# Kernel optimization log

Hardware: AMD Instinct MI355X
Metric: run time of the kernel (lower is better)

The kernel has to match this reference:

```python
import jax, jax.numpy as jnp
import numpy as np

N, P, T, D = 25000, 100000, 4, 128
DIN = 4 * D + 4  # 516
LEAKY = 0.001


def setup_inputs() -> dict:
    key = jax.random.key(0)
    ks = jax.random.split(key, 12)
    inp = {
        "coords": jax.random.normal(ks[0], (N, T, 3), jnp.float32),
        "propers": jax.random.randint(ks[1], (P, 4), 0, N, jnp.int64),
        "encoded": jax.random.normal(ks[2], (N, D), jnp.float32),
        "t": jax.random.uniform(ks[3], (T,), jnp.float32),
        "answer": jax.random.normal(ks[4], (N, T, 3), jnp.float32),
        # AggregateMLP(516 -> 128 -> 128 -> 128 -> 2), LeakyReLU(0.001) between
        "W0": jax.random.normal(ks[5], (DIN, D), jnp.float32) / np.sqrt(DIN),
        "b0": jnp.zeros((D,), jnp.float32),
        "W1": jax.random.normal(ks[6], (D, D), jnp.float32) / np.sqrt(D),
        "b1": jnp.zeros((D,), jnp.float32),
        "W2": jax.random.normal(ks[7], (D, D), jnp.float32) / np.sqrt(D),
        "b2": jnp.zeros((D,), jnp.float32),
        "W3": jax.random.normal(ks[8], (D, 2), jnp.float32) / np.sqrt(D),
        "b3": jnp.zeros((2,), jnp.float32),
    }
    return inp


def _forward(coords, propers, encoded, t, answer, W0, b0, W1, b1, W2, b2, W3, b3):
    p0, p1, p2, p3 = propers[:, 0], propers[:, 1], propers[:, 2], propers[:, 3]
    c0, c1, c2, c3 = coords[p0], coords[p1], coords[p2], coords[p3]  # [P,T,3]
    u1 = c1 - c0
    u2 = c2 - c1
    u3 = c3 - c2
    u1xu2 = jnp.cross(u1, u2, axis=-1)
    u2xu3 = jnp.cross(u2, u3, axis=-1)
    u2_norm = jnp.linalg.norm(u2, axis=-1, keepdims=True)
    u1yu2 = u1 * u2_norm
    theta = jnp.arctan2((u1yu2 * u2xu3).sum(-1), (u1xu2 * u2xu3).sum(-1))  # [P,T]
    dr = c0 - c3  # [P,T,3]
    dl = jnp.sqrt(jnp.clip(jnp.square(dr).sum(-1), 1e-12))  # [P,T]
    dh = dr / dl[..., None]

    Pn, Tn = propers.shape[0], t.shape[0]
    bcast = lambda e: jnp.broadcast_to(e[:, None, :], (Pn, Tn, e.shape[-1]))
    feats = jnp.concatenate(
        [
            bcast(encoded[p0]),
            bcast(encoded[p1]),
            bcast(encoded[p2]),
            bcast(encoded[p3]),
            jnp.broadcast_to(t.reshape(1, Tn, 1), (Pn, Tn, 1)),
            jnp.sin(theta)[..., None],
            jnp.cos(theta)[..., None],
            dl[..., None],
        ],
        axis=2,
    )  # [P,T,516]

    h = jax.nn.leaky_relu(feats @ W0 + b0, LEAKY)
    h = jax.nn.leaky_relu(h @ W1 + b1, LEAKY)
    h = jax.nn.leaky_relu(h @ W2 + b2, LEAKY)
    delta = h @ W3 + b3  # [P,T,2]

    out = answer.at[p0].add(-0.5 * delta[:, :, 0:1] * dh)
    out = out.at[p3].add(0.5 * delta[:, :, 1:2] * dh)
    return out


def reference(coords, propers, encoded, t, answer, W0, b0, W1, b1, W2, b2, W3, b3):
    return _forward(coords, propers, encoded, t, answer, W0, b0, W1, b1, W2, b2, W3, b3)
```

## Files before the change

kernel.cpp:

```cpp
#include <hip/hip_runtime.h>
#include <hip/hip_bf16.h>

#define NN 25000
#define PP 100000
#define TT 4
#define DD 128
#define LEAKY 0.001f

#define PB 16
#define ROWS 64

typedef __bf16 bf16;
typedef __bf16 bf16x8 __attribute__((ext_vector_type(8)));
typedef float  f32x4  __attribute__((ext_vector_type(4)));

#define OFF_ENCB  0u
#define OFF_W0SW  6400000u
#define OFF_W1SW  6531072u
#define OFF_W2SW  6563840u
#define OFF_W3SW  6596608u
#define WS_END    6600704u

#define PR_ENCB4 800000
#define PR_W0SW  65536
#define PR_W1SW  16384
#define PR_W2SW  16384
#define PR_W3SW  2048
#define PR_COPY4 75000
#define PR_TOTAL (PR_ENCB4 + PR_W0SW + PR_W1SW + PR_W2SW + PR_W3SW + PR_COPY4)

__global__ __launch_bounds__(256) void prep_kernel(
    const float* __restrict__ encoded, const float* __restrict__ W0,
    const float* __restrict__ W1, const float* __restrict__ W2,
    const float* __restrict__ W3, const float* __restrict__ answer,
    bf16* __restrict__ encB, bf16* __restrict__ W0sw, bf16* __restrict__ W1sw,
    bf16* __restrict__ W2sw, bf16* __restrict__ W3sw, float* __restrict__ out)
{
    int idx = blockIdx.x * 256 + threadIdx.x;
    if (idx < PR_ENCB4) {
        float4 v = ((const float4*)encoded)[idx];
        bf16 pk[4] = {(bf16)v.x, (bf16)v.y, (bf16)v.z, (bf16)v.w};
        *(uint2*)(encB + idx * 4) = *(const uint2*)pk;
        return;
    }
    idx -= PR_ENCB4;
    if (idx < PR_W0SW) {
        int j = idx & 7, lane = (idx >> 3) & 63, c = idx >> 9;
        int fr = lane & 15, quad = lane >> 4;
        int kc = c & 15, iwv = c >> 4;
        int k = kc * 32 + quad * 8 + j;
        W0sw[idx] = (bf16)W0[k * 128 + iwv * 16 + fr];
        return;
    }
    idx -= PR_W0SW;
    if (idx < PR_W1SW) {
        int j = idx & 7, lane = (idx >> 3) & 63, c = idx >> 9;
        int fr = lane & 15, quad = lane >> 4;
        int kc = c & 3, nt = c >> 2;
        int k = kc * 32 + quad * 8 + j;
        W1sw[idx] = (bf16)W1[k * 128 + nt * 16 + fr];
        return;
    }
    idx -= PR_W1SW;
    if (idx < PR_W2SW) {
        int j = idx & 7, lane = (idx >> 3) & 63, c = idx >> 9;
        int fr = lane & 15, quad = lane >> 4;
        int kc = c & 3, nt = c >> 2;
        int k = kc * 32 + quad * 8 + j;
        W2sw[idx] = (bf16)W2[k * 128 + nt * 16 + fr];
        return;
    }
    idx -= PR_W2SW;
    if (idx < PR_W3SW) {
        int j = idx & 7, lane = (idx >> 3) & 63, kc = idx >> 9;
        int fr = lane & 15, quad = lane >> 4;
        int k = kc * 32 + quad * 8 + j;
        W3sw[idx] = (fr < 2) ? (bf16)W3[k * 2 + fr] : (bf16)0.0f;
        return;
    }
    idx -= PR_W3SW;
    if (idx < PR_COPY4) { ((float4*)out)[idx] = ((const float4*)answer)[idx]; }
}

__global__ __launch_bounds__(256, 4) void main_kernel(
    const float* __restrict__ coords, const int* __restrict__ propers,
    const float* __restrict__ tvec, const float* __restrict__ W0,
    const float* __restrict__ b0, const float* __restrict__ b1,
    const float* __restrict__ b2, const float* __restrict__ b3,
    const bf16* __restrict__ encB, const bf16* __restrict__ W0sw,
    const bf16* __restrict__ W1sw, const bf16* __restrict__ W2sw,
    const bf16* __restrict__ W3sw, float* __restrict__ out)
{
    __shared__ bf16 sAH[8704];
    #define SA(p, c) sAH[(p) * 520 + (c)]
    #define SH(r, j) sAH[(r) * 136 + (j)]
    __shared__ int   sNodes[PB][4];
    __shared__ float sSn[ROWS], sCs[ROWS], sDl[ROWS], sDh[ROWS][3];
    __shared__ float sDelta[ROWS][2];

    const int tid  = threadIdx.x;
    const int pBase = blockIdx.x * PB;
    const float tv0 = tvec[0], tv1 = tvec[1], tv2 = tvec[2], tv3 = tvec[3];

    {
        int pair = tid >> 2, sg = tid & 3;
        int p = pair >> 2, i = pair & 3;
        int node = propers[(pBase + p) * 4 + i];
        if (sg == 0) sNodes[p][i] = node;
        const uint4* src = (const uint4*)(encB + (size_t)node * 128 + sg * 32);
        uint4* dst = (uint4*)(&SA(p, i * 128 + sg * 32));
        #pragma unroll
        for (int q = 0; q < 4; ++q) dst[q] = src[q];
    }
    if (tid < ROWS) {
        int r = tid, p = r >> 2, t = r & 3;
        const int* prow = propers + (pBase + p) * 4;
        int n0 = prow[0], n1 = prow[1], n2 = prow[2], n3 = prow[3];
        const float* c0 = coords + n0 * 12 + t * 3;
        const float* c1 = coords + n1 * 12 + t * 3;
        const float* c2 = coords + n2 * 12 + t * 3;
        const float* c3 = coords + n3 * 12 + t * 3;
        float u1x = c1[0]-c0[0], u1y = c1[1]-c0[1], u1z = c1[2]-c0[2];
        float u2x = c2[0]-c1[0], u2y = c2[1]-c1[1], u2z = c2[2]-c1[2];
        float u3x = c3[0]-c2[0], u3y = c3[1]-c2[1], u3z = c3[2]-c2[2];
        float ax = u1y*u2z - u1z*u2y, ay = u1z*u2x - u1x*u2z, az = u1x*u2y - u1y*u2x;
        float bx = u2y*u3z - u2z*u3y, by = u2z*u3x - u2x*u3z, bz = u2x*u3y - u2y*u3x;
        float u2n = sqrtf(u2x*u2x + u2y*u2y + u2z*u2z);
        float num = u2n * (u1x*bx + u1y*by + u1z*bz);
        float den = ax*bx + ay*by + az*bz;
        float hyp = sqrtf(num*num + den*den);
        float sn, cs;
        if (hyp > 1e-30f) { float ih = 1.0f / hyp; sn = num * ih; cs = den * ih; }
        else { sn = 0.0f; cs = 1.0f; }
        float drx = c0[0]-c3[0], dry = c0[1]-c3[1], drz = c0[2]-c3[2];
        float dl = sqrtf(fmaxf(drx*drx + dry*dry + drz*drz, 1e-12f));
        float il = 1.0f / dl;
        sSn[r] = sn; sCs[r] = cs; sDl[r] = dl;
        sDh[r][0] = drx * il; sDh[r][1] = dry * il; sDh[r][2] = drz * il;
    }
    __syncthreads();

    const int wv = tid >> 6, lane = tid & 63;
    const int fr = lane & 15;
    const int quad = lane >> 4;

    f32x4 acc0 = {0.f,0.f,0.f,0.f}, acc1 = {0.f,0.f,0.f,0.f};
    {
        const bf16* aBase = &SA(fr, quad * 8);
        const bf16* w0b = W0sw + (size_t)(wv * 2) * 16 * 512 + lane * 8;
        #pragma unroll
        for (int kc = 0; kc < 16; ++kc) {
            bf16x8 aF = *(const bf16x8*)(aBase + kc * 32);
            bf16x8 bF0 = *(const bf16x8*)(w0b + kc * 512);
            bf16x8 bF1 = *(const bf16x8*)(w0b + (16 + kc) * 512);
            acc0 = __builtin_amdgcn_mfma_f32_16x16x32_bf16(aF, bF0, acc0, 0, 0, 0);
            acc1 = __builtin_amdgcn_mfma_f32_16x16x32_bf16(aF, bF1, acc1, 0, 0, 0);
        }
    }
    __syncthreads();

    #pragma unroll
    for (int i = 0; i < 2; ++i) {
        int j = (wv * 2 + i) * 16 + fr;
        float w512 = W0[512 * 128 + j], w513 = W0[513 * 128 + j];
        float w514 = W0[514 * 128 + j], w515 = W0[515 * 128 + j];
        float bb = b0[j];
        const f32x4 acc = i ? acc1 : acc0;
        #pragma unroll
        for (int reg = 0; reg < 4; ++reg) {
            int p = quad * 4 + reg;
            float g = acc[reg];
            #pragma unroll
            for (int t = 0; t < 4; ++t) {
                int r = p * 4 + t;
                float tvv = (t == 0) ? tv0 : (t == 1) ? tv1 : (t == 2) ? tv2 : tv3;
                float v = g + tvv * w512 + sSn[r] * w513 + sCs[r] * w514 + sDl[r] * w515 + bb;
                v = v > 0.0f ? v : LEAKY * v;
                SH(r, j) = (bf16)v;
            }
        }
    }
    __syncthreads();

    f32x4 hacc[8];
    #pragma unroll
    for (int nt = 0; nt < 8; ++nt) hacc[nt] = (f32x4){0.f,0.f,0.f,0.f};
    {
        const bf16* aRow = &SH(wv * 16 + fr, quad * 8);
        const bf16* w1b = W1sw + lane * 8;
        #pragma unroll
        for (int kc = 0; kc < 4; ++kc) {
            bf16x8 aF = *(const bf16x8*)(aRow + kc * 32);
            #pragma unroll
            for (int nt = 0; nt < 8; ++nt) {
                bf16x8 bF = *(const bf16x8*)(w1b + (nt * 4 + kc) * 512);
                hacc[nt] = __builtin_amdgcn_mfma_f32_16x16x32_bf16(aF, bF, hacc[nt], 0, 0, 0);
            }
        }
    }
    __syncthreads();
    #pragma unroll
    for (int nt = 0; nt < 8; ++nt) {
        int j = nt * 16 + fr;
        float bb = b1[j];
        #pragma unroll
        for (int reg = 0; reg < 4; ++reg) {
            int r = wv * 16 + quad * 4 + reg;
            float v = hacc[nt][reg] + bb;
            v = v > 0.0f ? v : LEAKY * v;
            SH(r, j) = (bf16)v;
        }
    }
    __syncthreads();

    #pragma unroll
    for (int nt = 0; nt < 8; ++nt) hacc[nt] = (f32x4){0.f,0.f,0.f,0.f};
    {
        const bf16* aRow = &SH(wv * 16 + fr, quad * 8);
        const bf16* w2b = W2sw + lane * 8;
        #pragma unroll
        for (int kc = 0; kc < 4; ++kc) {
            bf16x8 aF = *(const bf16x8*)(aRow + kc * 32);
            #pragma unroll
            for (int nt = 0; nt < 8; ++nt) {
                bf16x8 bF = *(const bf16x8*)(w2b + (nt * 4 + kc) * 512);
                hacc[nt] = __builtin_amdgcn_mfma_f32_16x16x32_bf16(aF, bF, hacc[nt], 0, 0, 0);
            }
        }
    }
    __syncthreads();
    #pragma unroll
    for (int nt = 0; nt < 8; ++nt) {
        int j = nt * 16 + fr;
        float bb = b2[j];
        #pragma unroll
        for (int reg = 0; reg < 4; ++reg) {
            int r = wv * 16 + quad * 4 + reg;
            float v = hacc[nt][reg] + bb;
            v = v > 0.0f ? v : LEAKY * v;
            SH(r, j) = (bf16)v;
        }
    }
    __syncthreads();

    {
        f32x4 dacc = {0.f,0.f,0.f,0.f};
        const bf16* aRow = &SH(wv * 16 + fr, quad * 8);
        const bf16* w3b = W3sw + lane * 8;
        #pragma unroll
        for (int kc = 0; kc < 4; ++kc) {
            bf16x8 aF = *(const bf16x8*)(aRow + kc * 32);
            bf16x8 bF = *(const bf16x8*)(w3b + kc * 512);
            dacc = __builtin_amdgcn_mfma_f32_16x16x32_bf16(aF, bF, dacc, 0, 0, 0);
        }
        if (fr < 2) {
            float bb = b3[fr];
            #pragma unroll
            for (int reg = 0; reg < 4; ++reg)
                sDelta[wv * 16 + quad * 4 + reg][fr] = dacc[reg] + bb;
        }
    }
    __syncthreads();

    for (int idx = tid; idx < ROWS * 6; idx += 256) {
        int r = idx / 6, c = idx % 6;
        int p = r >> 2, t = r & 3;
        int side = c / 3, ax = c % 3;
        int node = sNodes[p][side ? 3 : 0];
        float dval = side ? 0.5f * sDelta[r][1] : -0.5f * sDelta[r][0];
        atomicAdd(out + node * 12 + t * 3 + ax, dval * sDh[r][ax]);
    }
    #undef SA
    #undef SH
}

extern "C" void kernel_launch(void* const* d_in, const int* in_sizes, int n_in,
                              void* d_out, int out_size, void* d_ws, size_t ws_size,
                              hipStream_t stream) {
    const float* coords  = (const float*)d_in[0];
    const int*   propers = (const int*)d_in[1];
    const float* encoded = (const float*)d_in[2];
    const float* tvec    = (const float*)d_in[3];
    const float* answer  = (const float*)d_in[4];
    const float* W0 = (const float*)d_in[5];
    const float* b0 = (const float*)d_in[6];
    const float* W1 = (const float*)d_in[7];
    const float* b1 = (const float*)d_in[8];
    const float* W2 = (const float*)d_in[9];
    const float* b2 = (const float*)d_in[10];
    const float* W3 = (const float*)d_in[11];
    const float* b3 = (const float*)d_in[12];
    float* out = (float*)d_out;
    char* ws = (char*)d_ws;
    bf16* encB = (bf16*)(ws + OFF_ENCB);
    bf16* W0sw = (bf16*)(ws + OFF_W0SW);
    bf16* W1sw = (bf16*)(ws + OFF_W1SW);
    bf16* W2sw = (bf16*)(ws + OFF_W2SW);
    bf16* W3sw = (bf16*)(ws + OFF_W3SW);

    int prep_blocks = (PR_TOTAL + 255) / 256;
    prep_kernel<<<prep_blocks, 256, 0, stream>>>(encoded, W0, W1, W2, W3, answer,
                                                 encB, W0sw, W1sw, W2sw, W3sw, out);
    main_kernel<<<PP / PB, 256, 0, stream>>>(coords, propers, tvec, W0, b0, b1, b2, b3,
                                             encB, W0sw, W1sw, W2sw, W3sw, out);
}
```

Baseline: 203.5 us.

## Double threads per block to 512 and split MLP tiles across eight waves

```diff
diff --git a/kernel.cpp b/kernel.cpp
--- a/kernel.cpp
+++ b/kernel.cpp
@@ -82,7 +82,7 @@
     if (idx < PR_COPY4) { ((float4*)out)[idx] = ((const float4*)answer)[idx]; }
 }
 
-__global__ __launch_bounds__(256, 4) void main_kernel(
+__global__ __launch_bounds__(512, 8) void main_kernel(
     const float* __restrict__ coords, const int* __restrict__ propers,
     const float* __restrict__ tvec, const float* __restrict__ W0,
     const float* __restrict__ b0, const float* __restrict__ b1,
@@ -103,14 +103,14 @@
     const float tv0 = tvec[0], tv1 = tvec[1], tv2 = tvec[2], tv3 = tvec[3];
 
     {
-        int pair = tid >> 2, sg = tid & 3;
-        int p = pair >> 2, i = pair & 3;
+        int row = tid >> 3, sg = tid & 7;
+        int p = row >> 2, i = row & 3;
         int node = propers[(pBase + p) * 4 + i];
         if (sg == 0) sNodes[p][i] = node;
-        const uint4* src = (const uint4*)(encB + (size_t)node * 128 + sg * 32);
-        uint4* dst = (uint4*)(&SA(p, i * 128 + sg * 32));
-        #pragma unroll
-        for (int q = 0; q < 4; ++q) dst[q] = src[q];
+        const uint4* src = (const uint4*)(encB + (size_t)node * 128 + sg * 16);
+        uint4* dst = (uint4*)(&SA(p, i * 128 + sg * 16));
+        dst[0] = src[0];
+        dst[1] = src[1];
     }
     if (tid < ROWS) {
         int r = tid, p = r >> 2, t = r & 3;
@@ -143,29 +143,27 @@
     const int wv = tid >> 6, lane = tid & 63;
     const int fr = lane & 15;
     const int quad = lane >> 4;
-
-    f32x4 acc0 = {0.f,0.f,0.f,0.f}, acc1 = {0.f,0.f,0.f,0.f};
+    const int m4 = wv & 3;
+    const int nh = wv >> 2;
+
+    f32x4 acc = {0.f,0.f,0.f,0.f};
     {
         const bf16* aBase = &SA(fr, quad * 8);
-        const bf16* w0b = W0sw + (size_t)(wv * 2) * 16 * 512 + lane * 8;
+        const bf16* w0b = W0sw + (size_t)wv * 16 * 512 + lane * 8;
         #pragma unroll
         for (int kc = 0; kc < 16; ++kc) {
             bf16x8 aF = *(const bf16x8*)(aBase + kc * 32);
-            bf16x8 bF0 = *(const bf16x8*)(w0b + kc * 512);
-            bf16x8 bF1 = *(const bf16x8*)(w0b + (16 + kc) * 512);
-            acc0 = __builtin_amdgcn_mfma_f32_16x16x32_bf16(aF, bF0, acc0, 0, 0, 0);
-            acc1 = __builtin_amdgcn_mfma_f32_16x16x32_bf16(aF, bF1, acc1, 0, 0, 0);
-        }
-    }
-    __syncthreads();
-
-    #pragma unroll
-    for (int i = 0; i < 2; ++i) {
-        int j = (wv * 2 + i) * 16 + fr;
+            bf16x8 bF = *(const bf16x8*)(w0b + kc * 512);
+            acc = __builtin_amdgcn_mfma_f32_16x16x32_bf16(aF, bF, acc, 0, 0, 0);
+        }
+    }
+    __syncthreads();
+
+    {
+        int j = wv * 16 + fr;
         float w512 = W0[512 * 128 + j], w513 = W0[513 * 128 + j];
         float w514 = W0[514 * 128 + j], w515 = W0[515 * 128 + j];
         float bb = b0[j];
-        const f32x4 acc = i ? acc1 : acc0;
         #pragma unroll
         for (int reg = 0; reg < 4; ++reg) {
             int p = quad * 4 + reg;
@@ -182,30 +180,30 @@
     }
     __syncthreads();
 
-    f32x4 hacc[8];
+    f32x4 hacc[4];
     #pragma unroll
-    for (int nt = 0; nt < 8; ++nt) hacc[nt] = (f32x4){0.f,0.f,0.f,0.f};
-    {
-        const bf16* aRow = &SH(wv * 16 + fr, quad * 8);
+    for (int nt = 0; nt < 4; ++nt) hacc[nt] = (f32x4){0.f,0.f,0.f,0.f};
+    {
+        const bf16* aRow = &SH(m4 * 16 + fr, quad * 8);
         const bf16* w1b = W1sw + lane * 8;
         #pragma unroll
         for (int kc = 0; kc < 4; ++kc) {
             bf16x8 aF = *(const bf16x8*)(aRow + kc * 32);
             #pragma unroll
-            for (int nt = 0; nt < 8; ++nt) {
-                bf16x8 bF = *(const bf16x8*)(w1b + (nt * 4 + kc) * 512);
+            for (int nt = 0; nt < 4; ++nt) {
+                bf16x8 bF = *(const bf16x8*)(w1b + ((nh * 4 + nt) * 4 + kc) * 512);
                 hacc[nt] = __builtin_amdgcn_mfma_f32_16x16x32_bf16(aF, bF, hacc[nt], 0, 0, 0);
             }
         }
     }
     __syncthreads();
     #pragma unroll
-    for (int nt = 0; nt < 8; ++nt) {
-        int j = nt * 16 + fr;
+    for (int nt = 0; nt < 4; ++nt) {
+        int j = (nh * 4 + nt) * 16 + fr;
         float bb = b1[j];
         #pragma unroll
         for (int reg = 0; reg < 4; ++reg) {
-            int r = wv * 16 + quad * 4 + reg;
+            int r = m4 * 16 + quad * 4 + reg;
             float v = hacc[nt][reg] + bb;
             v = v > 0.0f ? v : LEAKY * v;
             SH(r, j) = (bf16)v;
@@ -214,28 +212,28 @@
     __syncthreads();
 
     #pragma unroll
-    for (int nt = 0; nt < 8; ++nt) hacc[nt] = (f32x4){0.f,0.f,0.f,0.f};
-    {
-        const bf16* aRow = &SH(wv * 16 + fr, quad * 8);
+    for (int nt = 0; nt < 4; ++nt) hacc[nt] = (f32x4){0.f,0.f,0.f,0.f};
+    {
+        const bf16* aRow = &SH(m4 * 16 + fr, quad * 8);
         const bf16* w2b = W2sw + lane * 8;
         #pragma unroll
         for (int kc = 0; kc < 4; ++kc) {
             bf16x8 aF = *(const bf16x8*)(aRow + kc * 32);
             #pragma unroll
-            for (int nt = 0; nt < 8; ++nt) {
-                bf16x8 bF = *(const bf16x8*)(w2b + (nt * 4 + kc) * 512);
+            for (int nt = 0; nt < 4; ++nt) {
+                bf16x8 bF = *(const bf16x8*)(w2b + ((nh * 4 + nt) * 4 + kc) * 512);
                 hacc[nt] = __builtin_amdgcn_mfma_f32_16x16x32_bf16(aF, bF, hacc[nt], 0, 0, 0);
             }
         }
     }
     __syncthreads();
     #pragma unroll
-    for (int nt = 0; nt < 8; ++nt) {
-        int j = nt * 16 + fr;
+    for (int nt = 0; nt < 4; ++nt) {
+        int j = (nh * 4 + nt) * 16 + fr;
         float bb = b2[j];
         #pragma unroll
         for (int reg = 0; reg < 4; ++reg) {
-            int r = wv * 16 + quad * 4 + reg;
+            int r = m4 * 16 + quad * 4 + reg;
             float v = hacc[nt][reg] + bb;
             v = v > 0.0f ? v : LEAKY * v;
             SH(r, j) = (bf16)v;
@@ -243,7 +241,7 @@
     }
     __syncthreads();
 
-    {
+    if (wv < 4) {
         f32x4 dacc = {0.f,0.f,0.f,0.f};
         const bf16* aRow = &SH(wv * 16 + fr, quad * 8);
         const bf16* w3b = W3sw + lane * 8;
@@ -262,8 +260,8 @@
     }
     __syncthreads();
 
-    for (int idx = tid; idx < ROWS * 6; idx += 256) {
-        int r = idx / 6, c = idx % 6;
+    if (tid < ROWS * 6) {
+        int r = tid / 6, c = tid % 6;
         int p = r >> 2, t = r & 3;
         int side = c / 3, ax = c % 3;
         int node = sNodes[p][side ? 3 : 0];
@@ -301,6 +299,6 @@
     int prep_blocks = (PR_TOTAL + 255) / 256;
     prep_kernel<<<prep_blocks, 256, 0, stream>>>(encoded, W0, W1, W2, W3, answer,
                                                  encB, W0sw, W1sw, W2sw, W3sw, out);
-    main_kernel<<<PP / PB, 256, 0, stream>>>(coords, propers, tvec, W0, b0, b1, b2, b3,
+    main_kernel<<<PP / PB, 512, 0, stream>>>(coords, propers, tvec, W0, b0, b1, b2, b3,
                                              encB, W0sw, W1sw, W2sw, W3sw, out);
 }
```

New measurement: 197.6 us. 1.03x faster.
